# Kernel optimization log

Hardware: AMD Instinct MI355X
Metric: run time of the kernel (lower is better)

## Reference

```python
import jax, jax.numpy as jnp
import numpy as np

MARGIN = 0.3  # hard-coded in all three MarginRankingLoss instances


def setup_inputs() -> dict:
    key = jax.random.key(0)
    k1, k2, k3, k4 = jax.random.split(key, 4)
    n, d, num_ids = 4096, 2048, 100
    inputs = jax.random.normal(k1, (n, d), dtype=jnp.float32)
    targets_a = jax.random.randint(k2, (n,), 0, num_ids, dtype=jnp.int64)
    targets_b = jax.random.randint(k3, (n,), 0, num_ids, dtype=jnp.int64)
    lam = jax.random.uniform(k4, (), dtype=jnp.float32)
    epoch = 60
    return {"inputs": inputs, "targets_a": targets_a, "targets_b": targets_b,
            "lam": lam, "epoch": epoch}


def reference(inputs, targets_a, targets_b, lam, epoch):
    # pairwise euclidean distance: dist[i,j] = ||x_i - x_j||
    sq = jnp.sum(inputs * inputs, axis=1)                      # [n]
    dist = sq[:, None] + sq[None, :] - 2.0 * (inputs @ inputs.T)
    dist = jnp.sqrt(jnp.clip(dist, 1e-12))                     # [n, n]

    ma = targets_a[:, None] == targets_a[None, :]
    mb = targets_b[:, None] == targets_b[None, :]
    m_same_ab = ma & mb                                        # same a AND b (incl. diagonal)
    m_same_or = (ma & ~mb) | (~ma & mb)                        # exactly one of a/b matches
    m_dif_ab = ~ma & ~mb                                       # neither matches

    ninf = -jnp.inf
    pinf = jnp.inf
    hp = jnp.max(jnp.where(m_same_ab, dist, ninf), axis=1)     # hardest positive
    hn = jnp.min(jnp.where(m_dif_ab, dist, pinf), axis=1)      # hardest negative
    max_or = jnp.max(jnp.where(m_same_or, dist, ninf), axis=1)
    min_or = jnp.min(jnp.where(m_same_or, dist, pinf), axis=1)

    use_or = m_same_or.any(axis=1) & (epoch > 50)
    sp = jnp.where(use_or, max_or, hp)
    sn = jnp.where(use_or, min_or, hn)

    # MarginRankingLoss(x1, x2, y=1) = mean(relu(x2 - x1 + margin))
    loss_1 = jnp.mean(jnp.maximum(0.0, hp - hn + MARGIN))
    loss_2 = jnp.mean(jnp.maximum(0.0, sp - hn + MARGIN))
    loss_3 = jnp.mean(jnp.maximum(0.0, hp - sn + MARGIN))
    return loss_1 + loss_2 + loss_3
```

## Files before the change

kernel.cpp:

```cpp
#include <hip/hip_runtime.h>
#include <hip/hip_bf16.h>

#define NROW 4096
#define KDIM 2048
#define ROWB (KDIM * 2)
#define BT 128
#define NB (NROW / BT)
#define BK 32
#define NT (KDIM / BK)
#define KTBUF 16384
#define AB_OFF 8192
#define PHI(r) ((((r) >> 1) & 3) << 4)

typedef __attribute__((ext_vector_type(8))) short bf16x8;
typedef __attribute__((ext_vector_type(4))) float f32x4;
typedef __attribute__((ext_vector_type(4))) unsigned short u16x4;

#define MFMA16(a, b, c) __builtin_amdgcn_mfma_f32_16x16x32_bf16((a), (b), (c), 0, 0, 0)

__device__ __forceinline__ unsigned short f2bf(float x) {
    unsigned u = __float_as_uint(x);
    unsigned r = (u + 0x7FFFu + ((u >> 16) & 1u)) >> 16;
    return (unsigned short)r;
}
__device__ __forceinline__ float bf2f(unsigned short b) {
    return __uint_as_float(((unsigned)b) << 16);
}

__global__ __launch_bounds__(256) void k_convert(const float* __restrict__ X,
                                                 unsigned short* __restrict__ Xb,
                                                 float* __restrict__ sqv,
                                                 unsigned* __restrict__ hp,
                                                 unsigned* __restrict__ hn,
                                                 unsigned* __restrict__ mor,
                                                 unsigned* __restrict__ mir,
                                                 float* __restrict__ out) {
    const int row = blockIdx.x;
    const int t = threadIdx.x;
    if (row < 16) {
        const int i = row * 256 + t;
        hp[i] = 0u;
        hn[i] = 0x7F800000u;
        mor[i] = 0u;
        mir[i] = 0x7F800000u;
        if (i == 0) out[0] = 0.f;
    }
    const float4* xr = (const float4*)(X + (size_t)row * KDIM);
    unsigned short* br = Xb + (size_t)row * KDIM;
    float acc = 0.f;
#pragma unroll
    for (int it = 0; it < 2; ++it) {
        int idx = t * 2 + it;
        float4 v = xr[idx];
        u16x4 b;
        b.x = f2bf(v.x); b.y = f2bf(v.y); b.z = f2bf(v.z); b.w = f2bf(v.w);
        float f0 = bf2f(b.x), f1 = bf2f(b.y), f2 = bf2f(b.z), f3 = bf2f(b.w);
        acc += f0 * f0 + f1 * f1 + f2 * f2 + f3 * f3;
        *(u16x4*)(br + idx * 4) = b;
    }
#pragma unroll
    for (int s = 32; s > 0; s >>= 1) acc += __shfl_xor(acc, s);
    __shared__ float red[4];
    const int lane = t & 63, wid = t >> 6;
    if (lane == 0) red[wid] = acc;
    __syncthreads();
    if (t == 0) sqv[row] = red[0] + red[1] + red[2] + red[3];
}

__global__ __launch_bounds__(512, 4) void k_gemm(const unsigned short* __restrict__ Xb,
                                                 const float* __restrict__ sqv,
                                                 const int* __restrict__ ta,
                                                 const int* __restrict__ tb,
                                                 unsigned int* __restrict__ hp,
                                                 unsigned int* __restrict__ hn,
                                                 unsigned int* __restrict__ mor,
                                                 unsigned int* __restrict__ mir) {
    __shared__ char lds[3 * KTBUF];
    int rem = blockIdx.x;
    int bi = 0;
    while (rem >= NB - bi) { rem -= NB - bi; ++bi; }
    const int bj = bi + rem;

    const int t = threadIdx.x;
    const int lane = t & 63;
    const int w = t >> 6;
    const int wm = w >> 2;
    const int wn = w & 3;
    const int l15 = lane & 15;
    const int kg16 = (lane >> 4) * 16;
    const char* xbase = (const char*)Xb;

    const int swz = ((l15 >> 1) & 3) << 4;
    const int akbase = (wm * 64 + l15) * 64 + (kg16 ^ swz);
    const int bkbase = AB_OFF + (wn * 32 + l15) * 64 + (kg16 ^ swz);

    f32x4 acc[4][2] = {};

#define STAGE(tt, sb3)                                                        \
    do {                                                                      \
        _Pragma("unroll")                                                     \
        for (int isb_ = 0; isb_ < 2; ++isb_) {                                \
            const int row_ = t >> 2;                                          \
            const int gr_ = (isb_ ? bj : bi) * BT + row_;                     \
            const char* gsrc_ = xbase + (size_t)gr_ * ROWB +                  \
                                (size_t)(tt) * 64 +                           \
                                (((t & 3) * 16) ^ PHI(row_));                 \
            char* ldst_ = lds + (sb3) * KTBUF + isb_ * AB_OFF +               \
                          row_ * 64 + (t & 3) * 16;                           \
            __builtin_amdgcn_global_load_lds(                                 \
                (const __attribute__((address_space(1))) void*)gsrc_,         \
                (__attribute__((address_space(3))) void*)ldst_, 16, 0, 0);    \
        }                                                                     \
    } while (0)

    STAGE(0, 0);
    STAGE(1, 1);

    int r3 = 0, s3 = 2;
    for (int tk = 0; tk < NT; ++tk) {
        if (tk < NT - 1)
            asm volatile("s_waitcnt vmcnt(2)" ::: "memory");
        else
            asm volatile("s_waitcnt vmcnt(0)" ::: "memory");
        __builtin_amdgcn_s_barrier();

        const char* buf = lds + r3 * KTBUF;
        bf16x8 af[4], bfr[2];
#pragma unroll
        for (int m = 0; m < 4; ++m)
            af[m] = *(const bf16x8*)(buf + akbase + m * 1024);
#pragma unroll
        for (int n = 0; n < 2; ++n)
            bfr[n] = *(const bf16x8*)(buf + bkbase + n * 1024);

        if (tk + 2 < NT) STAGE(tk + 2, s3);

#pragma unroll
        for (int m = 0; m < 4; ++m)
#pragma unroll
            for (int n = 0; n < 2; ++n)
                acc[m][n] = MFMA16(af[m], bfr[n], acc[m][n]);

        r3 = (r3 == 2) ? 0 : r3 + 1;
        s3 = (s3 == 2) ? 0 : s3 + 1;
    }
#undef STAGE

    float sqj[2];
    int taj[2], tbj[2];
#pragma unroll
    for (int n = 0; n < 2; ++n) {
        int j = bj * BT + wn * 32 + n * 16 + l15;
        sqj[n] = sqv[j];
        taj[n] = ta[j];
        tbj[n] = tb[j];
    }
    const float INF = __uint_as_float(0x7F800000u);

    float chp[2], chn[2], cmo[2], cmi[2];
#pragma unroll
    for (int n = 0; n < 2; ++n) {
        chp[n] = 0.f; chn[n] = INF; cmo[n] = 0.f; cmi[n] = INF;
    }

#pragma unroll
    for (int m = 0; m < 4; ++m) {
#pragma unroll
        for (int reg = 0; reg < 4; ++reg) {
            const int i = bi * BT + wm * 64 + m * 16 + (lane >> 4) * 4 + reg;
            const float sqi = sqv[i];
            const int tai = ta[i], tbi = tb[i];
            float vhp = 0.f, vhn = INF, vmo = 0.f, vmi = INF;
#pragma unroll
            for (int n = 0; n < 2; ++n) {
                float d2 = fmaxf(sqi + sqj[n] - 2.f * acc[m][n][reg], 1e-12f);
                bool ma = (tai == taj[n]), mb = (tbi == tbj[n]);
                if (ma && mb) {
                    vhp = fmaxf(vhp, d2);
                    chp[n] = fmaxf(chp[n], d2);
                } else if (ma != mb) {
                    vmo = fmaxf(vmo, d2);
                    vmi = fminf(vmi, d2);
                    cmo[n] = fmaxf(cmo[n], d2);
                    cmi[n] = fminf(cmi[n], d2);
                } else {
                    vhn = fminf(vhn, d2);
                    chn[n] = fminf(chn[n], d2);
                }
            }
#pragma unroll
            for (int s = 1; s < 16; s <<= 1) {
                vhp = fmaxf(vhp, __shfl_xor(vhp, s, 16));
                vhn = fminf(vhn, __shfl_xor(vhn, s, 16));
                vmo = fmaxf(vmo, __shfl_xor(vmo, s, 16));
                vmi = fminf(vmi, __shfl_xor(vmi, s, 16));
            }
            if (l15 == 0) {
                if (vhp > 0.f) atomicMax(&hp[i], __float_as_uint(vhp));
                if (vhn < INF) atomicMin(&hn[i], __float_as_uint(vhn));
                if (vmo > 0.f) {
                    atomicMax(&mor[i], __float_as_uint(vmo));
                    atomicMin(&mir[i], __float_as_uint(vmi));
                }
            }
        }
    }

    if (bi != bj) {
#pragma unroll
        for (int n = 0; n < 2; ++n) {
            float a = chp[n], b = chn[n], c = cmo[n], d = cmi[n];
            a = fmaxf(a, __shfl_xor(a, 16)); a = fmaxf(a, __shfl_xor(a, 32));
            b = fminf(b, __shfl_xor(b, 16)); b = fminf(b, __shfl_xor(b, 32));
            c = fmaxf(c, __shfl_xor(c, 16)); c = fmaxf(c, __shfl_xor(c, 32));
            d = fminf(d, __shfl_xor(d, 16)); d = fminf(d, __shfl_xor(d, 32));
            if (lane < 16) {
                const int j = bj * BT + wn * 32 + n * 16 + lane;
                if (a > 0.f) atomicMax(&hp[j], __float_as_uint(a));
                if (b < INF) atomicMin(&hn[j], __float_as_uint(b));
                if (c > 0.f) {
                    atomicMax(&mor[j], __float_as_uint(c));
                    atomicMin(&mir[j], __float_as_uint(d));
                }
            }
        }
    }
}

__global__ __launch_bounds__(256) void k_final(const unsigned* __restrict__ hp,
                                               const unsigned* __restrict__ hn,
                                               const unsigned* __restrict__ mor,
                                               const unsigned* __restrict__ mir,
                                               const int* __restrict__ epoch_p,
                                               float* __restrict__ out) {
    const int t = threadIdx.x;
    const int i = blockIdx.x * 256 + t;
    const bool eok = (*epoch_p > 50);
    const unsigned morb = mor[i];
    float fhp = sqrtf(__uint_as_float(hp[i]));
    float fhn = sqrtf(__uint_as_float(hn[i]));
    bool use_or = (morb != 0u) && eok;
    float sp = use_or ? sqrtf(__uint_as_float(morb)) : fhp;
    float sn = use_or ? sqrtf(__uint_as_float(mir[i])) : fhn;
    float s = fmaxf(0.f, fhp - fhn + 0.3f) + fmaxf(0.f, sp - fhn + 0.3f) +
              fmaxf(0.f, fhp - sn + 0.3f);
#pragma unroll
    for (int sh = 32; sh > 0; sh >>= 1) s += __shfl_xor(s, sh);
    __shared__ float red[4];
    const int lane = t & 63, wid = t >> 6;
    if (lane == 0) red[wid] = s;
    __syncthreads();
    if (t == 0)
        atomicAdd(out, (red[0] + red[1] + red[2] + red[3]) * (1.f / 4096.f));
}

extern "C" void kernel_launch(void* const* d_in, const int* in_sizes, int n_in,
                              void* d_out, int out_size, void* d_ws, size_t ws_size,
                              hipStream_t stream) {
    const float* X = (const float*)d_in[0];
    const int* ta = (const int*)d_in[1];
    const int* tb = (const int*)d_in[2];
    const int* epoch_p = (const int*)d_in[4];
    float* out = (float*)d_out;

    char* ws = (char*)d_ws;
    unsigned short* Xb = (unsigned short*)ws;
    size_t off = (size_t)NROW * KDIM * sizeof(unsigned short);
    float* sqv = (float*)(ws + off); off += (size_t)NROW * 4;
    unsigned* hp = (unsigned*)(ws + off); off += (size_t)NROW * 4;
    unsigned* hn = (unsigned*)(ws + off); off += (size_t)NROW * 4;
    unsigned* mor = (unsigned*)(ws + off); off += (size_t)NROW * 4;
    unsigned* mir = (unsigned*)(ws + off); off += (size_t)NROW * 4;

    k_convert<<<NROW, 256, 0, stream>>>(X, Xb, sqv, hp, hn, mor, mir, out);
    k_gemm<<<(NB * (NB + 1)) / 2, 512, 0, stream>>>(Xb, sqv, ta, tb,
                                                    hp, hn, mor, mir);
    k_final<<<NROW / 256, 256, 0, stream>>>(hp, hn, mor, mir, epoch_p, out);
}
```

Baseline: 97.06 us.

## Split GEMM tiles into 128x64 blocks with two waves of 64x64 each

The symmetric distance GEMM now uses 128x64 output tiles, with two blocks per upper-triangular tile pair, and 128-thread blocks. Each wave computes a 64x64 sub-tile instead of 64x32, so more MFMA work is done per LDS fragment load. The grid doubles and the per-stage LDS buffer shrinks. Each thread issues six async global-to-LDS loads per stage, and the vmcnt wait is adjusted to match. The trade-off is far fewer waves per CU for hiding latency, plus higher register pressure from the 4x4 accumulator array.

```diff
diff --git a/kernel.cpp b/kernel.cpp
--- a/kernel.cpp
+++ b/kernel.cpp
@@ -4,11 +4,12 @@
 #define NROW 4096
 #define KDIM 2048
 #define ROWB (KDIM * 2)
-#define BT 128
-#define NB (NROW / BT)
+#define BTM 128
+#define BTN 64
+#define NB (NROW / BTM)
 #define BK 32
 #define NT (KDIM / BK)
-#define KTBUF 16384
+#define KTBUF 12288
 #define AB_OFF 8192
 #define PHI(r) ((((r) >> 1) & 3) << 4)
 
@@ -67,7 +68,7 @@
     if (t == 0) sqv[row] = red[0] + red[1] + red[2] + red[3];
 }
 
-__global__ __launch_bounds__(512, 4) void k_gemm(const unsigned short* __restrict__ Xb,
+__global__ __launch_bounds__(128, 2) void k_gemm(const unsigned short* __restrict__ Xb,
                                                  const float* __restrict__ sqv,
                                                  const int* __restrict__ ta,
                                                  const int* __restrict__ tb,
@@ -76,7 +77,8 @@
                                                  unsigned int* __restrict__ mor,
                                                  unsigned int* __restrict__ mir) {
     __shared__ char lds[3 * KTBUF];
-    int rem = blockIdx.x;
+    int rem = blockIdx.x >> 1;
+    const int h = blockIdx.x & 1;
     int bi = 0;
     while (rem >= NB - bi) { rem -= NB - bi; ++bi; }
     const int bj = bi + rem;
@@ -84,29 +86,39 @@
     const int t = threadIdx.x;
     const int lane = t & 63;
     const int w = t >> 6;
-    const int wm = w >> 2;
-    const int wn = w & 3;
     const int l15 = lane & 15;
     const int kg16 = (lane >> 4) * 16;
     const char* xbase = (const char*)Xb;
 
     const int swz = ((l15 >> 1) & 3) << 4;
-    const int akbase = (wm * 64 + l15) * 64 + (kg16 ^ swz);
-    const int bkbase = AB_OFF + (wn * 32 + l15) * 64 + (kg16 ^ swz);
-
-    f32x4 acc[4][2] = {};
+    const int akbase = (w * 64 + l15) * 64 + (kg16 ^ swz);
+    const int bkbase = AB_OFF + l15 * 64 + (kg16 ^ swz);
+
+    f32x4 acc[4][4] = {};
 
 #define STAGE(tt, sb3)                                                        \
     do {                                                                      \
         _Pragma("unroll")                                                     \
-        for (int isb_ = 0; isb_ < 2; ++isb_) {                                \
-            const int row_ = t >> 2;                                          \
-            const int gr_ = (isb_ ? bj : bi) * BT + row_;                     \
+        for (int c_ = 0; c_ < 4; ++c_) {                                      \
+            const int row_ = c_ * 32 + (t >> 2);                              \
+            const int gr_ = bi * BTM + row_;                                  \
             const char* gsrc_ = xbase + (size_t)gr_ * ROWB +                  \
                                 (size_t)(tt) * 64 +                           \
                                 (((t & 3) * 16) ^ PHI(row_));                 \
-            char* ldst_ = lds + (sb3) * KTBUF + isb_ * AB_OFF +               \
-                          row_ * 64 + (t & 3) * 16;                           \
+            char* ldst_ = lds + (sb3) * KTBUF + row_ * 64 + (t & 3) * 16;     \
+            __builtin_amdgcn_global_load_lds(                                 \
+                (const __attribute__((address_space(1))) void*)gsrc_,         \
+                (__attribute__((address_space(3))) void*)ldst_, 16, 0, 0);    \
+        }                                                                     \
+        _Pragma("unroll")                                                     \
+        for (int c_ = 0; c_ < 2; ++c_) {                                      \
+            const int row_ = c_ * 32 + (t >> 2);                              \
+            const int gr_ = bj * BTM + h * BTN + row_;                        \
+            const char* gsrc_ = xbase + (size_t)gr_ * ROWB +                  \
+                                (size_t)(tt) * 64 +                           \
+                                (((t & 3) * 16) ^ PHI(row_));                 \
+            char* ldst_ = lds + (sb3) * KTBUF + AB_OFF + row_ * 64 +          \
+                          (t & 3) * 16;                                       \
             __builtin_amdgcn_global_load_lds(                                 \
                 (const __attribute__((address_space(1))) void*)gsrc_,         \
                 (__attribute__((address_space(3))) void*)ldst_, 16, 0, 0);    \
@@ -119,18 +131,18 @@
     int r3 = 0, s3 = 2;
     for (int tk = 0; tk < NT; ++tk) {
         if (tk < NT - 1)
-            asm volatile("s_waitcnt vmcnt(2)" ::: "memory");
+            asm volatile("s_waitcnt vmcnt(6)" ::: "memory");
         else
             asm volatile("s_waitcnt vmcnt(0)" ::: "memory");
         __builtin_amdgcn_s_barrier();
 
         const char* buf = lds + r3 * KTBUF;
-        bf16x8 af[4], bfr[2];
+        bf16x8 af[4], bfr[4];
 #pragma unroll
         for (int m = 0; m < 4; ++m)
             af[m] = *(const bf16x8*)(buf + akbase + m * 1024);
 #pragma unroll
-        for (int n = 0; n < 2; ++n)
+        for (int n = 0; n < 4; ++n)
             bfr[n] = *(const bf16x8*)(buf + bkbase + n * 1024);
 
         if (tk + 2 < NT) STAGE(tk + 2, s3);
@@ -138,7 +150,7 @@
 #pragma unroll
         for (int m = 0; m < 4; ++m)
 #pragma unroll
-            for (int n = 0; n < 2; ++n)
+            for (int n = 0; n < 4; ++n)
                 acc[m][n] = MFMA16(af[m], bfr[n], acc[m][n]);
 
         r3 = (r3 == 2) ? 0 : r3 + 1;
@@ -146,20 +158,20 @@
     }
 #undef STAGE
 
-    float sqj[2];
-    int taj[2], tbj[2];
-#pragma unroll
-    for (int n = 0; n < 2; ++n) {
-        int j = bj * BT + wn * 32 + n * 16 + l15;
+    float sqj[4];
+    int taj[4], tbj[4];
+#pragma unroll
+    for (int n = 0; n < 4; ++n) {
+        int j = bj * BTM + h * BTN + n * 16 + l15;
         sqj[n] = sqv[j];
         taj[n] = ta[j];
         tbj[n] = tb[j];
     }
     const float INF = __uint_as_float(0x7F800000u);
 
-    float chp[2], chn[2], cmo[2], cmi[2];
-#pragma unroll
-    for (int n = 0; n < 2; ++n) {
+    float chp[4], chn[4], cmo[4], cmi[4];
+#pragma unroll
+    for (int n = 0; n < 4; ++n) {
         chp[n] = 0.f; chn[n] = INF; cmo[n] = 0.f; cmi[n] = INF;
     }
 
@@ -167,12 +179,12 @@
     for (int m = 0; m < 4; ++m) {
 #pragma unroll
         for (int reg = 0; reg < 4; ++reg) {
-            const int i = bi * BT + wm * 64 + m * 16 + (lane >> 4) * 4 + reg;
+            const int i = bi * BTM + w * 64 + m * 16 + (lane >> 4) * 4 + reg;
             const float sqi = sqv[i];
             const int tai = ta[i], tbi = tb[i];
             float vhp = 0.f, vhn = INF, vmo = 0.f, vmi = INF;
 #pragma unroll
-            for (int n = 0; n < 2; ++n) {
+            for (int n = 0; n < 4; ++n) {
                 float d2 = fmaxf(sqi + sqj[n] - 2.f * acc[m][n][reg], 1e-12f);
                 bool ma = (tai == taj[n]), mb = (tbi == tbj[n]);
                 if (ma && mb) {
@@ -208,14 +220,14 @@
 
     if (bi != bj) {
 #pragma unroll
-        for (int n = 0; n < 2; ++n) {
+        for (int n = 0; n < 4; ++n) {
             float a = chp[n], b = chn[n], c = cmo[n], d = cmi[n];
             a = fmaxf(a, __shfl_xor(a, 16)); a = fmaxf(a, __shfl_xor(a, 32));
             b = fminf(b, __shfl_xor(b, 16)); b = fminf(b, __shfl_xor(b, 32));
             c = fmaxf(c, __shfl_xor(c, 16)); c = fmaxf(c, __shfl_xor(c, 32));
             d = fminf(d, __shfl_xor(d, 16)); d = fminf(d, __shfl_xor(d, 32));
             if (lane < 16) {
-                const int j = bj * BT + wn * 32 + n * 16 + lane;
+                const int j = bj * BTM + h * BTN + n * 16 + lane;
                 if (a > 0.f) atomicMax(&hp[j], __float_as_uint(a));
                 if (b < INF) atomicMin(&hn[j], __float_as_uint(b));
                 if (c > 0.f) {
@@ -273,7 +285,7 @@
     unsigned* mir = (unsigned*)(ws + off); off += (size_t)NROW * 4;
 
     k_convert<<<NROW, 256, 0, stream>>>(X, Xb, sqv, hp, hn, mor, mir, out);
-    k_gemm<<<(NB * (NB + 1)) / 2, 512, 0, stream>>>(Xb, sqv, ta, tb,
-                                                    hp, hn, mor, mir);
+    k_gemm<<<NB * (NB + 1), 128, 0, stream>>>(Xb, sqv, ta, tb,
+                                              hp, hn, mor, mir);
     k_final<<<NROW / 256, 256, 0, stream>>>(hp, hn, mor, mir, epoch_p, out);
 }
```

New measurement: 112.1 us. +15.5%, slower.
